# Kernel tuning notes

Hardware: AMD Instinct MI355X
Metric: run time of the kernel (lower is better)

## Reference

```python
import jax, jax.numpy as jnp
import numpy as np

EPS = 1e-5  # BatchNorm eps

def conv1x1(x, w, b):
    # x: [B,C,H,W], w: [O,C], b: [O]
    return jnp.einsum('bchw,oc->bohw', x, w) + b[None, :, None, None]

def bn(x, s, b, m, v):
    # eval-mode BatchNorm2d with running stats m,v
    inv = s * jax.lax.rsqrt(v + EPS)
    return x * inv[None, :, None, None] + (b - m * inv)[None, :, None, None]

def maxpool2(x):
    B, C, H, W = x.shape
    return x.reshape(B, C, H // 2, 2, W // 2, 2).max(axis=(3, 5))

def setup_inputs() -> dict:
    key = jax.random.key(0)
    ks = jax.random.split(key, 32)
    B, CH, H, W = 8, 64, 64, 64
    cq, cv = CH // 8, CH // 2
    r = lambda k, sh: jax.random.normal(k, sh, dtype=jnp.float32)
    u = lambda k, sh: jax.random.uniform(k, sh, dtype=jnp.float32)
    return {
        'x': r(ks[0], (B, CH, H, W)),
        'memory': r(ks[1], (B, CH, H, W)),
        'wq': r(ks[2], (cq, CH)) * 0.1, 'bq': r(ks[3], (cq,)) * 0.1,
        'bnq_s': u(ks[4], (cq,)), 'bnq_b': r(ks[5], (cq,)) * 0.1,
        'bnq_m': r(ks[6], (cq,)) * 0.1, 'bnq_v': u(ks[7], (cq,)),
        'wk': r(ks[8], (cq, CH)) * 0.1, 'bk': r(ks[9], (cq,)) * 0.1,
        'bnk_s': u(ks[10], (cq,)), 'bnk_b': r(ks[11], (cq,)) * 0.1,
        'bnk_m': r(ks[12], (cq,)) * 0.1, 'bnk_v': u(ks[13], (cq,)),
        'wv': r(ks[14], (cv, CH)) * 0.1, 'bv': r(ks[15], (cv,)) * 0.1,
        'bnv_s': u(ks[16], (cv,)), 'bnv_b': r(ks[17], (cv,)) * 0.1,
        'bnv_m': r(ks[18], (cv,)) * 0.1, 'bnv_v': u(ks[19], (cv,)),
        'wp': r(ks[20], (CH, cv)) * 0.1, 'bp': r(ks[21], (CH,)) * 0.1,
        'bnp_s': u(ks[22], (CH,)), 'bnp_b': r(ks[23], (CH,)) * 0.1,
        'bnp_m': r(ks[24], (CH,)) * 0.1, 'bnp_v': u(ks[25], (CH,)),
        'gamma': r(ks[26], (1,)),
    }

def reference(x, memory, wq, bq, bnq_s, bnq_b, bnq_m, bnq_v,
              wk, bk, bnk_s, bnk_b, bnk_m, bnk_v,
              wv, bv, bnv_s, bnv_b, bnv_m, bnv_v,
              wp, bp, bnp_s, bnp_b, bnp_m, bnp_v, gamma):
    B, CH, H, W = x.shape
    cq, cv = CH // 8, CH // 2
    HW, HW4 = H * W, (H * W) // 4
    # query from full-res memory: [B, HW, cq]
    q = bn(conv1x1(memory, wq, bq), bnq_s, bnq_b, bnq_m, bnq_v)
    q = q.reshape(B, cq, HW).transpose(0, 2, 1)
    # key pooled: [B, cq, HW/4]
    k = maxpool2(bn(conv1x1(memory, wk, bk), bnk_s, bnk_b, bnk_m, bnk_v))
    k = k.reshape(B, cq, HW4)
    # attention: [B, HW, HW/4], softmax over last dim (no scaling, as in source)
    attn = jax.nn.softmax(jnp.einsum('bnc,bcm->bnm', q, k), axis=2)
    # value pooled: [B, HW/4, cv]
    v = maxpool2(bn(conv1x1(memory, wv, bv), bnv_s, bnv_b, bnv_m, bnv_v))
    v = v.reshape(B, cv, HW4).transpose(0, 2, 1)
    # attn_g: [B, HW, cv] -> [B, cv, H, W]
    g = jnp.einsum('bnm,bmc->bnc', attn, v).transpose(0, 2, 1).reshape(B, cv, H, W)
    g = bn(conv1x1(g, wp, bp), bnp_s, bnp_b, bnp_m, bnp_v)
    return x + gamma * g
```

## Files before the change

### kernel.cpp

```cpp
#include <hip/hip_runtime.h>

#define EPS_BN 1e-5f

constexpr int Bn   = 8;
constexpr int CHn  = 64;
constexpr int HWn  = 4096;
constexpr int HW4n = 1024;
constexpr int CQn  = 8;
constexpr int CVn  = 32;

typedef short bf16x8 __attribute__((ext_vector_type(8)));
typedef float f32x4  __attribute__((ext_vector_type(4)));

union FragI { int4 i; bf16x8 v; };

__device__ __forceinline__ unsigned short f2bf(float f) {
    unsigned u = __float_as_uint(f);
    unsigned r = u + 0x7FFFu + ((u >> 16) & 1u);
    return (unsigned short)(r >> 16);
}
__device__ __forceinline__ float bf2f(unsigned short h) {
    return __uint_as_float(((unsigned)h) << 16);
}

__device__ __align__(16) short g_Kh[Bn * HW4n * CQn];
__device__ __align__(16) short g_Kl[Bn * HW4n * CQn];
__device__ __align__(16) short g_Vt[Bn * CVn * HW4n];

__global__ __launch_bounds__(192)
void k_proj_kv(const float* __restrict__ mem,
               const float* __restrict__ wk,  const float* __restrict__ bk,
               const float* __restrict__ ks,  const float* __restrict__ kb,
               const float* __restrict__ km,  const float* __restrict__ kv,
               const float* __restrict__ wv,  const float* __restrict__ bv_,
               const float* __restrict__ vs,  const float* __restrict__ vb,
               const float* __restrict__ vm,  const float* __restrict__ vv)
{
    __shared__ float wall[2560];
    __shared__ float beta[40];
    __shared__ float Msh[8192];

    const int tid = threadIdx.x;
    for (int idx = tid; idx < 2560; idx += 192) {
        int c = idx % 40, ch = idx / 40;
        float w, inv;
        if (c < 8) { inv = ks[c] * rsqrtf(kv[c] + EPS_BN); w = wk[c * 64 + ch]; }
        else { int c2 = c - 8; inv = vs[c2] * rsqrtf(vv[c2] + EPS_BN); w = wv[c2 * 64 + ch]; }
        wall[ch * 40 + c] = w * inv;
    }
    if (tid < 40) {
        int c = tid;
        if (c < 8) {
            float inv = ks[c] * rsqrtf(kv[c] + EPS_BN);
            beta[c] = (bk[c] - km[c]) * inv + kb[c];
        } else {
            int c2 = c - 8;
            float inv = vs[c2] * rsqrtf(vv[c2] + EPS_BN);
            beta[c] = (bv_[c2] - vm[c2]) * inv + vb[c2];
        }
    }

    const int b = blockIdx.x >> 5;
    const int R = blockIdx.x & 31;

    {
        const float* src = mem + (size_t)b * (CHn * HWn) + (R << 7);
        for (int idx = tid; idx < 4096; idx += 192) {
            int ch = idx >> 6, p2 = idx & 63;
            float2 v = *(const float2*)(src + ch * HWn + (p2 << 1));
            int r = p2 >> 5, w2 = p2 & 31;
            *(float2*)&Msh[ch * 128 + (w2 << 2) + (r << 1)] = v;
        }
    }
    __syncthreads();

    if (tid < 160) {
        const int g  = tid % 5;
        const int qd = tid / 5;
        float acc[4][8];
        #pragma unroll
        for (int p = 0; p < 4; ++p)
            #pragma unroll
            for (int c = 0; c < 8; ++c) acc[p][c] = 0.f;

        for (int ch = 0; ch < 64; ++ch) {
            const float4 mq = *(const float4*)&Msh[ch * 128 + (qd << 2)];
            const float4* wr = (const float4*)&wall[ch * 40 + (g << 3)];
            const float4 w0 = wr[0], w1 = wr[1];
            #pragma unroll
            for (int p = 0; p < 4; ++p) {
                const float mv = (p == 0) ? mq.x : (p == 1) ? mq.y : (p == 2) ? mq.z : mq.w;
                acc[p][0] = fmaf(w0.x, mv, acc[p][0]); acc[p][1] = fmaf(w0.y, mv, acc[p][1]);
                acc[p][2] = fmaf(w0.z, mv, acc[p][2]); acc[p][3] = fmaf(w0.w, mv, acc[p][3]);
                acc[p][4] = fmaf(w1.x, mv, acc[p][4]); acc[p][5] = fmaf(w1.y, mv, acc[p][5]);
                acc[p][6] = fmaf(w1.z, mv, acc[p][6]); acc[p][7] = fmaf(w1.w, mv, acc[p][7]);
            }
        }
        float o[8];
        #pragma unroll
        for (int c = 0; c < 8; ++c)
            o[c] = fmaxf(fmaxf(acc[0][c], acc[1][c]), fmaxf(acc[2][c], acc[3][c]))
                 + beta[(g << 3) + c];

        const int m = (R << 5) + qd;
        if (g == 0) {
            unsigned short hb[8], lb[8];
            #pragma unroll
            for (int c = 0; c < 8; ++c) {
                hb[c] = f2bf(o[c]);
                lb[c] = f2bf(o[c] - bf2f(hb[c]));
            }
            int4 hi4 = make_int4((int)(hb[0] | ((unsigned)hb[1] << 16)),
                                 (int)(hb[2] | ((unsigned)hb[3] << 16)),
                                 (int)(hb[4] | ((unsigned)hb[5] << 16)),
                                 (int)(hb[6] | ((unsigned)hb[7] << 16)));
            int4 lo4 = make_int4((int)(lb[0] | ((unsigned)lb[1] << 16)),
                                 (int)(lb[2] | ((unsigned)lb[3] << 16)),
                                 (int)(lb[4] | ((unsigned)lb[5] << 16)),
                                 (int)(lb[6] | ((unsigned)lb[7] << 16)));
            *(int4*)&g_Kh[((size_t)b * HW4n + m) * CQn] = hi4;
            *(int4*)&g_Kl[((size_t)b * HW4n + m) * CQn] = lo4;
        } else {
            const int ch0 = (g - 1) << 3;
            #pragma unroll
            for (int c = 0; c < 8; ++c)
                g_Vt[(size_t)b * (CVn * HW4n) + (ch0 + c) * HW4n + m] = (short)f2bf(o[c]);
        }
    }
}

__global__ __launch_bounds__(256, 2)
void k_attn6(const float* __restrict__ mem,
             const float* __restrict__ x,
             const float* __restrict__ wq, const float* __restrict__ bq,
             const float* __restrict__ qs, const float* __restrict__ qb,
             const float* __restrict__ qm, const float* __restrict__ qv,
             const float* __restrict__ wp, const float* __restrict__ bp,
             const float* __restrict__ ps, const float* __restrict__ pb,
             const float* __restrict__ pm, const float* __restrict__ pv,
             const float* __restrict__ gamma,
             float* __restrict__ out)
{
    __shared__ __align__(16) short Kh_sh[HW4n * CQn];
    __shared__ __align__(16) short Kl_sh[HW4n * CQn];
    __shared__ __align__(16) short Vt_sh[32 * 264];
    __shared__ __align__(16) short Psh[4 * 16 * 40];
    __shared__ __align__(16) float qw_sh[512];
    __shared__ float qbeta_sh[8];
    __shared__ float pbeta_sh[64];

    const int tid  = threadIdx.x;
    const int lane = tid & 63;
    const int w    = tid >> 6;
    const int quad = lane >> 4;
    const int c    = lane & 15;
    const int b    = blockIdx.x >> 6;
    const int tile = blockIdx.x & 63;
    const float gm = gamma[0];

    for (int idx = tid; idx < 512; idx += 256) {
        int cc = idx & 7, ch = idx >> 3;
        float inv = qs[cc] * rsqrtf(qv[cc] + EPS_BN);
        qw_sh[ch * 8 + cc] = wq[cc * 64 + ch] * inv;
    }
    if (tid < 8) {
        float inv = qs[tid] * rsqrtf(qv[tid] + EPS_BN);
        qbeta_sh[tid] = (bq[tid] - qm[tid]) * inv + qb[tid];
    }
    if (tid < 64) {
        float inv = ps[tid] * rsqrtf(pv[tid] + EPS_BN);
        pbeta_sh[tid] = gm * ((bp[tid] - pm[tid]) * inv + pb[tid]);
    }
    {
        const int4* Kh4 = (const int4*)(g_Kh + (size_t)b * (HW4n * CQn));
        const int4* Kl4 = (const int4*)(g_Kl + (size_t)b * (HW4n * CQn));
        int4* dh = (int4*)Kh_sh;
        int4* dl = (int4*)Kl_sh;
        #pragma unroll
        for (int i = 0; i < 4; ++i) {
            dh[tid + i * 256] = Kh4[tid + i * 256];
            dl[tid + i * 256] = Kl4[tid + i * 256];
        }
        const short* Vsrc = g_Vt + (size_t)b * (CVn * HW4n);
        #pragma unroll
        for (int i = 0; i < 4; ++i) {
            int idx4 = tid + i * 256;
            int ch = idx4 >> 5, ko = (idx4 & 31) << 3;
            *(int4*)&Vt_sh[ch * 264 + ko] = *(const int4*)(Vsrc + ch * HW4n + ko);
        }
    }
    __syncthreads();

    float q0 = 0.f, q1 = 0.f, q2 = 0.f, q3 = 0.f, q4 = 0.f, q5 = 0.f, q6 = 0.f, q7 = 0.f;
    {
        const float* mp = mem + (size_t)b * (CHn * HWn) + (tile << 6) + (w << 4) + c;
        #pragma unroll
        for (int cc = 0; cc < 16; ++cc) {
            const int ch = (quad << 4) | cc;
            const float mv = mp[ch * HWn];
            const float4 w0 = *(const float4*)&qw_sh[ch * 8];
            const float4 w1 = *(const float4*)&qw_sh[ch * 8 + 4];
            q0 = fmaf(w0.x, mv, q0); q1 = fmaf(w0.y, mv, q1);
            q2 = fmaf(w0.z, mv, q2); q3 = fmaf(w0.w, mv, q3);
            q4 = fmaf(w1.x, mv, q4); q5 = fmaf(w1.y, mv, q5);
            q6 = fmaf(w1.z, mv, q6); q7 = fmaf(w1.w, mv, q7);
        }
        q0 += __shfl_xor(q0, 16); q0 += __shfl_xor(q0, 32); q0 += qbeta_sh[0];
        q1 += __shfl_xor(q1, 16); q1 += __shfl_xor(q1, 32); q1 += qbeta_sh[1];
        q2 += __shfl_xor(q2, 16); q2 += __shfl_xor(q2, 32); q2 += qbeta_sh[2];
        q3 += __shfl_xor(q3, 16); q3 += __shfl_xor(q3, 32); q3 += qbeta_sh[3];
        q4 += __shfl_xor(q4, 16); q4 += __shfl_xor(q4, 32); q4 += qbeta_sh[4];
        q5 += __shfl_xor(q5, 16); q5 += __shfl_xor(q5, 32); q5 += qbeta_sh[5];
        q6 += __shfl_xor(q6, 16); q6 += __shfl_xor(q6, 32); q6 += qbeta_sh[6];
        q7 += __shfl_xor(q7, 16); q7 += __shfl_xor(q7, 32); q7 += qbeta_sh[7];
    }
    bf16x8 bqh, bql;
    {
        unsigned short h0 = f2bf(q0), h1 = f2bf(q1), h2 = f2bf(q2), h3 = f2bf(q3);
        unsigned short h4 = f2bf(q4), h5 = f2bf(q5), h6 = f2bf(q6), h7 = f2bf(q7);
        unsigned short l0 = f2bf(q0 - bf2f(h0)), l1 = f2bf(q1 - bf2f(h1));
        unsigned short l2 = f2bf(q2 - bf2f(h2)), l3 = f2bf(q3 - bf2f(h3));
        unsigned short l4 = f2bf(q4 - bf2f(h4)), l5 = f2bf(q5 - bf2f(h5));
        unsigned short l6 = f2bf(q6 - bf2f(h6)), l7 = f2bf(q7 - bf2f(h7));
        FragI fh, fl;
        fh.i = make_int4((int)(h0 | ((unsigned)h1 << 16)), (int)(h2 | ((unsigned)h3 << 16)),
                         (int)(h4 | ((unsigned)h5 << 16)), (int)(h6 | ((unsigned)h7 << 16)));
        fl.i = make_int4((int)(l0 | ((unsigned)l1 << 16)), (int)(l2 | ((unsigned)l3 << 16)),
                         (int)(l4 | ((unsigned)l5 << 16)), (int)(l6 | ((unsigned)l7 << 16)));
        FragI fz; fz.i = make_int4(0, 0, 0, 0);
        bqh = (quad == 0) ? fh.v : fz.v;
        bql = (quad == 0) ? fl.v : fz.v;
    }

    f32x4 acc0 = {0.f, 0.f, 0.f, 0.f};
    f32x4 acc1 = {0.f, 0.f, 0.f, 0.f};
    float m_ = -3.0e38f, l_ = 0.f;

    const int pbase = w * 640 + c * 40;
    const int pread = w * 640 + c * 40 + (quad << 3);

    for (int chunk = 0; chunk < 4; ++chunk) {
        if (chunk) {
            __syncthreads();
            const short* Vsrc = g_Vt + (size_t)b * (CVn * HW4n) + (chunk << 8);
            #pragma unroll
            for (int i = 0; i < 4; ++i) {
                int idx4 = tid + i * 256;
                int ch = idx4 >> 5, ko = (idx4 & 31) << 3;
                *(int4*)&Vt_sh[ch * 264 + ko] = *(const int4*)(Vsrc + ch * HW4n + ko);
            }
            __syncthreads();
        }
        for (int st = 0; st < 8; ++st) {
            const int kb   = (chunk << 8) + (st << 5);
            const int kloc = st << 5;

            f32x4 sa = {0.f, 0.f, 0.f, 0.f};
            f32x4 sb = {0.f, 0.f, 0.f, 0.f};
            {
                const bf16x8 ah0 = *(const bf16x8*)&Kh_sh[(kb + c) * 8];
                const bf16x8 al0 = *(const bf16x8*)&Kl_sh[(kb + c) * 8];
                sa = __builtin_amdgcn_mfma_f32_16x16x32_bf16(ah0, bqh, sa, 0, 0, 0);
                sa = __builtin_amdgcn_mfma_f32_16x16x32_bf16(ah0, bql, sa, 0, 0, 0);
                sa = __builtin_amdgcn_mfma_f32_16x16x32_bf16(al0, bqh, sa, 0, 0, 0);
                const bf16x8 ah1 = *(const bf16x8*)&Kh_sh[(kb + 16 + c) * 8];
                const bf16x8 al1 = *(const bf16x8*)&Kl_sh[(kb + 16 + c) * 8];
                sb = __builtin_amdgcn_mfma_f32_16x16x32_bf16(ah1, bqh, sb, 0, 0, 0);
                sb = __builtin_amdgcn_mfma_f32_16x16x32_bf16(ah1, bql, sb, 0, 0, 0);
                sb = __builtin_amdgcn_mfma_f32_16x16x32_bf16(al1, bqh, sb, 0, 0, 0);
            }

            float mx = fmaxf(fmaxf(fmaxf(sa[0], sa[1]), fmaxf(sa[2], sa[3])),
                             fmaxf(fmaxf(sb[0], sb[1]), fmaxf(sb[2], sb[3])));
            mx = fmaxf(mx, m_);
            mx = fmaxf(mx, __shfl_xor(mx, 16));
            mx = fmaxf(mx, __shfl_xor(mx, 32));
            const float alpha = __expf(m_ - mx);
            m_ = mx;
            const float pa0 = __expf(sa[0] - mx), pa1 = __expf(sa[1] - mx);
            const float pa2 = __expf(sa[2] - mx), pa3 = __expf(sa[3] - mx);
            const float pb0 = __expf(sb[0] - mx), pb1 = __expf(sb[1] - mx);
            const float pb2 = __expf(sb[2] - mx), pb3 = __expf(sb[3] - mx);
            l_ = l_ * alpha + (pa0 + pa1 + pa2 + pa3 + pb0 + pb1 + pb2 + pb3);

            *(int*)&Psh[pbase + (quad << 2)]          = (int)(f2bf(pa0) | ((unsigned)f2bf(pa1) << 16));
            *(int*)&Psh[pbase + (quad << 2) + 2]      = (int)(f2bf(pa2) | ((unsigned)f2bf(pa3) << 16));
            *(int*)&Psh[pbase + 16 + (quad << 2)]     = (int)(f2bf(pb0) | ((unsigned)f2bf(pb1) << 16));
            *(int*)&Psh[pbase + 16 + (quad << 2) + 2] = (int)(f2bf(pb2) | ((unsigned)f2bf(pb3) << 16));

            const float a0 = __shfl(alpha, 20 * quad + 0);
            const float a1 = __shfl(alpha, 20 * quad + 1);
            const float a2 = __shfl(alpha, 20 * quad + 2);
            const float a3 = __shfl(alpha, 20 * quad + 3);
            acc0[0] *= a0; acc0[1] *= a1; acc0[2] *= a2; acc0[3] *= a3;
            acc1[0] *= a0; acc1[1] *= a1; acc1[2] *= a2; acc1[3] *= a3;

            const bf16x8 pfrag = *(const bf16x8*)&Psh[pread];
            const bf16x8 v0 = *(const bf16x8*)&Vt_sh[c * 264 + kloc + (quad << 3)];
            const bf16x8 v1 = *(const bf16x8*)&Vt_sh[(16 + c) * 264 + kloc + (quad << 3)];
            acc0 = __builtin_amdgcn_mfma_f32_16x16x32_bf16(pfrag, v0, acc0, 0, 0, 0);
            acc1 = __builtin_amdgcn_mfma_f32_16x16x32_bf16(pfrag, v1, acc1, 0, 0, 0);
        }
    }

    __syncthreads();

    float* wpf = (float*)Vt_sh;
    for (int idx = tid; idx < 2048; idx += 256) {
        int o = idx >> 5, cc = idx & 31;
        float inv = ps[o] * rsqrtf(pv[o] + EPS_BN);
        wpf[o * 36 + cc] = wp[o * 32 + cc] * inv * gm;
    }

    {
        l_ += __shfl_xor(l_, 16);
        l_ += __shfl_xor(l_, 32);
        const float rl = 1.0f / l_;
        const float r0 = __shfl(rl, 20 * quad + 0);
        const float r1 = __shfl(rl, 20 * quad + 1);
        const float r2 = __shfl(rl, 20 * quad + 2);
        const float r3 = __shfl(rl, 20 * quad + 3);
        float* Gsh = (float*)Kh_sh;
        const int row = (w << 4) + (quad << 2);
        Gsh[(row + 0) * 36 + c] = acc0[0] * r0;
        Gsh[(row + 1) * 36 + c] = acc0[1] * r1;
        Gsh[(row + 2) * 36 + c] = acc0[2] * r2;
        Gsh[(row + 3) * 36 + c] = acc0[3] * r3;
        Gsh[(row + 0) * 36 + 16 + c] = acc1[0] * r0;
        Gsh[(row + 1) * 36 + 16 + c] = acc1[1] * r1;
        Gsh[(row + 2) * 36 + 16 + c] = acc1[2] * r2;
        Gsh[(row + 3) * 36 + 16 + c] = acc1[3] * r3;
    }
    __syncthreads();

    {
        const float* Gsh = (const float*)Kh_sh;
        const int q = tid >> 2, r = tid & 3;
        const float4* gq4 = (const float4*)&Gsh[q * 36];
        float g[32];
        #pragma unroll
        for (int i = 0; i < 8; ++i) {
            const float4 gv = gq4[i];
            g[4*i+0] = gv.x; g[4*i+1] = gv.y; g[4*i+2] = gv.z; g[4*i+3] = gv.w;
        }
        const int n = (tile << 6) + q;
        const float* xp = x + (size_t)b * (CHn * HWn) + n;
        float* op = out + (size_t)b * (CHn * HWn) + n;

        #pragma unroll
        for (int oo = 0; oo < 16; ++oo) {
            const int o = (oo << 2) | r;
            const float4* wr = (const float4*)&wpf[o * 36];
            float po = pbeta_sh[o];
            #pragma unroll
            for (int c4 = 0; c4 < 8; ++c4) {
                const float4 ww = wr[c4];
                po += ww.x * g[4*c4] + ww.y * g[4*c4+1] + ww.z * g[4*c4+2] + ww.w * g[4*c4+3];
            }
            op[o * HWn] = xp[o * HWn] + po;
        }
    }
}

extern "C" void kernel_launch(void* const* d_in, const int* in_sizes, int n_in,
                              void* d_out, int out_size, void* d_ws, size_t ws_size,
                              hipStream_t stream)
{
    const float* x    = (const float*)d_in[0];
    const float* mem  = (const float*)d_in[1];
    const float* wq   = (const float*)d_in[2];
    const float* bq   = (const float*)d_in[3];
    const float* bnqs = (const float*)d_in[4];
    const float* bnqb = (const float*)d_in[5];
    const float* bnqm = (const float*)d_in[6];
    const float* bnqv = (const float*)d_in[7];
    const float* wk   = (const float*)d_in[8];
    const float* bk   = (const float*)d_in[9];
    const float* bnks = (const float*)d_in[10];
    const float* bnkb = (const float*)d_in[11];
    const float* bnkm = (const float*)d_in[12];
    const float* bnkv = (const float*)d_in[13];
    const float* wv   = (const float*)d_in[14];
    const float* bv   = (const float*)d_in[15];
    const float* bnvs = (const float*)d_in[16];
    const float* bnvb = (const float*)d_in[17];
    const float* bnvm = (const float*)d_in[18];
    const float* bnvv = (const float*)d_in[19];
    const float* wp   = (const float*)d_in[20];
    const float* bp   = (const float*)d_in[21];
    const float* bnps = (const float*)d_in[22];
    const float* bnpb = (const float*)d_in[23];
    const float* bnpm = (const float*)d_in[24];
    const float* bnpv = (const float*)d_in[25];
    const float* gam  = (const float*)d_in[26];

    (void)d_ws; (void)ws_size; (void)in_sizes; (void)n_in; (void)out_size;

    k_proj_kv<<<dim3(256), dim3(192), 0, stream>>>(mem,
        wk, bk, bnks, bnkb, bnkm, bnkv,
        wv, bv, bnvs, bnvb, bnvm, bnvv);
    k_attn6<<<dim3(512), dim3(256), 0, stream>>>(mem, x,
        wq, bq, bnqs, bnqb, bnqm, bnqv,
        wp, bp, bnps, bnpb, bnpm, bnpv, gam,
        (float*)d_out);
}
```

Before: 159.9 us.

## Pack split-bf16 QK into one MFMA and double-buffer V tiles

The hi/lo split-bf16 QK product is now computed with one MFMA per 16 keys instead of three. Each lane quad selects a different Kh/Kl row and qh/ql fragment, so the 32-wide K dimension holds all four cross terms. V staging uses smaller 128-key chunks in a double-buffered shared array: the next chunk is loaded while the current one is consumed, leaving one barrier per chunk instead of two. The P scratch buffer is also double-buffered and the kernel is pinned to 2 waves per EU; the extra lo*lo term and the new synchronization pattern change accuracy slightly and need correct barrier placement.

```diff
diff --git a/kernel.cpp b/kernel.cpp
--- a/kernel.cpp
+++ b/kernel.cpp
@@ -129,8 +129,8 @@
     }
 }
 
-__global__ __launch_bounds__(256, 2)
-void k_attn6(const float* __restrict__ mem,
+__global__ __launch_bounds__(256, 2) __attribute__((amdgpu_waves_per_eu(2, 2)))
+void k_attn7(const float* __restrict__ mem,
              const float* __restrict__ x,
              const float* __restrict__ wq, const float* __restrict__ bq,
              const float* __restrict__ qs, const float* __restrict__ qb,
@@ -143,8 +143,8 @@
 {
     __shared__ __align__(16) short Kh_sh[HW4n * CQn];
     __shared__ __align__(16) short Kl_sh[HW4n * CQn];
-    __shared__ __align__(16) short Vt_sh[32 * 264];
-    __shared__ __align__(16) short Psh[4 * 16 * 40];
+    __shared__ __align__(16) short Vt_sh[2][32 * 136];
+    __shared__ __align__(16) short Psh[2][4 * 16 * 40];
     __shared__ __align__(16) float qw_sh[512];
     __shared__ float qbeta_sh[8];
     __shared__ float pbeta_sh[64];
@@ -171,6 +171,7 @@
         float inv = ps[tid] * rsqrtf(pv[tid] + EPS_BN);
         pbeta_sh[tid] = gm * ((bp[tid] - pm[tid]) * inv + pb[tid]);
     }
+    const short* Vsrc = g_Vt + (size_t)b * (CVn * HW4n);
     {
         const int4* Kh4 = (const int4*)(g_Kh + (size_t)b * (HW4n * CQn));
         const int4* Kl4 = (const int4*)(g_Kl + (size_t)b * (HW4n * CQn));
@@ -181,12 +182,11 @@
             dh[tid + i * 256] = Kh4[tid + i * 256];
             dl[tid + i * 256] = Kl4[tid + i * 256];
         }
-        const short* Vsrc = g_Vt + (size_t)b * (CVn * HW4n);
-        #pragma unroll
-        for (int i = 0; i < 4; ++i) {
-            int idx4 = tid + i * 256;
-            int ch = idx4 >> 5, ko = (idx4 & 31) << 3;
-            *(int4*)&Vt_sh[ch * 264 + ko] = *(const int4*)(Vsrc + ch * HW4n + ko);
+        #pragma unroll
+        for (int i = 0; i < 2; ++i) {
+            int idx4 = tid + (i << 8);
+            int ch = idx4 >> 4, k8 = idx4 & 15;
+            *(int4*)&Vt_sh[0][ch * 136 + (k8 << 3)] = *(const int4*)(Vsrc + ch * HW4n + (k8 << 3));
         }
     }
     __syncthreads();
@@ -214,7 +214,7 @@
         q6 += __shfl_xor(q6, 16); q6 += __shfl_xor(q6, 32); q6 += qbeta_sh[6];
         q7 += __shfl_xor(q7, 16); q7 += __shfl_xor(q7, 32); q7 += qbeta_sh[7];
     }
-    bf16x8 bqh, bql;
+    bf16x8 bqsel;
     {
         unsigned short h0 = f2bf(q0), h1 = f2bf(q1), h2 = f2bf(q2), h3 = f2bf(q3);
         unsigned short h4 = f2bf(q4), h5 = f2bf(q5), h6 = f2bf(q6), h7 = f2bf(q7);
@@ -227,10 +227,9 @@
                          (int)(h4 | ((unsigned)h5 << 16)), (int)(h6 | ((unsigned)h7 << 16)));
         fl.i = make_int4((int)(l0 | ((unsigned)l1 << 16)), (int)(l2 | ((unsigned)l3 << 16)),
                          (int)(l4 | ((unsigned)l5 << 16)), (int)(l6 | ((unsigned)l7 << 16)));
-        FragI fz; fz.i = make_int4(0, 0, 0, 0);
-        bqh = (quad == 0) ? fh.v : fz.v;
-        bql = (quad == 0) ? fl.v : fz.v;
-    }
+        bqsel = (quad & 1) ? fl.v : fh.v;
+    }
+    const short* Krow = (quad < 2) ? Kh_sh : Kl_sh;
 
     f32x4 acc0 = {0.f, 0.f, 0.f, 0.f};
     f32x4 acc1 = {0.f, 0.f, 0.f, 0.f};
@@ -239,35 +238,30 @@
     const int pbase = w * 640 + c * 40;
     const int pread = w * 640 + c * 40 + (quad << 3);
 
-    for (int chunk = 0; chunk < 4; ++chunk) {
-        if (chunk) {
-            __syncthreads();
-            const short* Vsrc = g_Vt + (size_t)b * (CVn * HW4n) + (chunk << 8);
-            #pragma unroll
-            for (int i = 0; i < 4; ++i) {
-                int idx4 = tid + i * 256;
-                int ch = idx4 >> 5, ko = (idx4 & 31) << 3;
-                *(int4*)&Vt_sh[ch * 264 + ko] = *(const int4*)(Vsrc + ch * HW4n + ko);
-            }
-            __syncthreads();
-        }
-        for (int st = 0; st < 8; ++st) {
-            const int kb   = (chunk << 8) + (st << 5);
+    for (int chunk = 0; chunk < 8; ++chunk) {
+        const int cur = chunk & 1;
+        if (chunk < 7) {
+            const short* Vn = Vsrc + ((chunk + 1) << 7);
+            #pragma unroll
+            for (int i = 0; i < 2; ++i) {
+                int idx4 = tid + (i << 8);
+                int ch = idx4 >> 4, k8 = idx4 & 15;
+                *(int4*)&Vt_sh[cur ^ 1][ch * 136 + (k8 << 3)] = *(const int4*)(Vn + ch * HW4n + (k8 << 3));
+            }
+        }
+        #pragma unroll
+        for (int st = 0; st < 4; ++st) {
+            const int kb   = (chunk << 7) + (st << 5);
             const int kloc = st << 5;
+            const int pbuf = st & 1;
 
             f32x4 sa = {0.f, 0.f, 0.f, 0.f};
             f32x4 sb = {0.f, 0.f, 0.f, 0.f};
             {
-                const bf16x8 ah0 = *(const bf16x8*)&Kh_sh[(kb + c) * 8];
-                const bf16x8 al0 = *(const bf16x8*)&Kl_sh[(kb + c) * 8];
-                sa = __builtin_amdgcn_mfma_f32_16x16x32_bf16(ah0, bqh, sa, 0, 0, 0);
-                sa = __builtin_amdgcn_mfma_f32_16x16x32_bf16(ah0, bql, sa, 0, 0, 0);
-                sa = __builtin_amdgcn_mfma_f32_16x16x32_bf16(al0, bqh, sa, 0, 0, 0);
-                const bf16x8 ah1 = *(const bf16x8*)&Kh_sh[(kb + 16 + c) * 8];
-                const bf16x8 al1 = *(const bf16x8*)&Kl_sh[(kb + 16 + c) * 8];
-                sb = __builtin_amdgcn_mfma_f32_16x16x32_bf16(ah1, bqh, sb, 0, 0, 0);
-                sb = __builtin_amdgcn_mfma_f32_16x16x32_bf16(ah1, bql, sb, 0, 0, 0);
-                sb = __builtin_amdgcn_mfma_f32_16x16x32_bf16(al1, bqh, sb, 0, 0, 0);
+                const bf16x8 a0 = *(const bf16x8*)&Krow[(kb + c) * 8];
+                sa = __builtin_amdgcn_mfma_f32_16x16x32_bf16(a0, bqsel, sa, 0, 0, 0);
+                const bf16x8 a1 = *(const bf16x8*)&Krow[(kb + 16 + c) * 8];
+                sb = __builtin_amdgcn_mfma_f32_16x16x32_bf16(a1, bqsel, sb, 0, 0, 0);
             }
 
             float mx = fmaxf(fmaxf(fmaxf(sa[0], sa[1]), fmaxf(sa[2], sa[3])),
@@ -283,10 +277,10 @@
             const float pb2 = __expf(sb[2] - mx), pb3 = __expf(sb[3] - mx);
             l_ = l_ * alpha + (pa0 + pa1 + pa2 + pa3 + pb0 + pb1 + pb2 + pb3);
 
-            *(int*)&Psh[pbase + (quad << 2)]          = (int)(f2bf(pa0) | ((unsigned)f2bf(pa1) << 16));
-            *(int*)&Psh[pbase + (quad << 2) + 2]      = (int)(f2bf(pa2) | ((unsigned)f2bf(pa3) << 16));
-            *(int*)&Psh[pbase + 16 + (quad << 2)]     = (int)(f2bf(pb0) | ((unsigned)f2bf(pb1) << 16));
-            *(int*)&Psh[pbase + 16 + (quad << 2) + 2] = (int)(f2bf(pb2) | ((unsigned)f2bf(pb3) << 16));
+            *(int*)&Psh[pbuf][pbase + (quad << 2)]          = (int)(f2bf(pa0) | ((unsigned)f2bf(pa1) << 16));
+            *(int*)&Psh[pbuf][pbase + (quad << 2) + 2]      = (int)(f2bf(pa2) | ((unsigned)f2bf(pa3) << 16));
+            *(int*)&Psh[pbuf][pbase + 16 + (quad << 2)]     = (int)(f2bf(pb0) | ((unsigned)f2bf(pb1) << 16));
+            *(int*)&Psh[pbuf][pbase + 16 + (quad << 2) + 2] = (int)(f2bf(pb2) | ((unsigned)f2bf(pb3) << 16));
 
             const float a0 = __shfl(alpha, 20 * quad + 0);
             const float a1 = __shfl(alpha, 20 * quad + 1);
@@ -295,15 +289,14 @@
             acc0[0] *= a0; acc0[1] *= a1; acc0[2] *= a2; acc0[3] *= a3;
             acc1[0] *= a0; acc1[1] *= a1; acc1[2] *= a2; acc1[3] *= a3;
 
-            const bf16x8 pfrag = *(const bf16x8*)&Psh[pread];
-            const bf16x8 v0 = *(const bf16x8*)&Vt_sh[c * 264 + kloc + (quad << 3)];
-            const bf16x8 v1 = *(const bf16x8*)&Vt_sh[(16 + c) * 264 + kloc + (quad << 3)];
+            const bf16x8 pfrag = *(const bf16x8*)&Psh[pbuf][pread];
+            const bf16x8 v0 = *(const bf16x8*)&Vt_sh[cur][c * 136 + kloc + (quad << 3)];
+            const bf16x8 v1 = *(const bf16x8*)&Vt_sh[cur][(16 + c) * 136 + kloc + (quad << 3)];
             acc0 = __builtin_amdgcn_mfma_f32_16x16x32_bf16(pfrag, v0, acc0, 0, 0, 0);
             acc1 = __builtin_amdgcn_mfma_f32_16x16x32_bf16(pfrag, v1, acc1, 0, 0, 0);
         }
-    }
-
-    __syncthreads();
+        __syncthreads();
+    }
 
     float* wpf = (float*)Vt_sh;
     for (int idx = tid; idx < 2048; idx += 256) {
@@ -399,7 +392,7 @@
     k_proj_kv<<<dim3(256), dim3(192), 0, stream>>>(mem,
         wk, bk, bnks, bnkb, bnkm, bnkv,
         wv, bv, bnvs, bnvb, bnvm, bnvv);
-    k_attn6<<<dim3(512), dim3(256), 0, stream>>>(mem, x,
+    k_attn7<<<dim3(512), dim3(256), 0, stream>>>(mem, x,
         wq, bq, bnqs, bnqb, bnqm, bnqv,
         wp, bp, bnps, bnpb, bnpm, bnpv, gam,
         (float*)d_out);
```

After: 154.4 us. -3.4%, faster.
